# Optimization experiments

Measured on AMD Instinct MI355X. Metric: run time of the kernel, lower is better.

## Reference

```python
import jax, jax.numpy as jnp
import numpy as np

N = 6144
D_LAT = 512


def setup_inputs() -> dict:
    key = jax.random.key(0)
    k1, k2, k3 = jax.random.split(key, 3)
    latent = jax.random.normal(k1, (N, D_LAT), dtype=jnp.float32)
    coords = jax.random.normal(k2, (N, 3), dtype=jnp.float32)
    alpha = jax.random.uniform(k3, (N,), dtype=jnp.float32)
    return {"latent": latent, "coords": coords, "alpha": alpha}


def reference(latent, coords, alpha):
    # Pairwise Euclidean distances via the Gram trick (avoids [N,N,3] diff tensor).
    sq = jnp.sum(coords * coords, axis=-1)                      # [N]
    d2 = sq[:, None] + sq[None, :] - 2.0 * (coords @ coords.T)  # [N,N]
    # max with tiny eps keeps sqrt grad finite on the (zeroed-out) diagonal
    D = jnp.sqrt(jnp.maximum(d2, 1e-12)) + 1e-6                 # [N,N]
    a = 0.5 * (alpha[:, None] + alpha[None, :])                 # [N,N]
    K = jnp.clip(jnp.power(D, -a), 1e-8, 1000.0) * jnp.exp(-D / 12.0)
    K = K * (1.0 - jnp.eye(K.shape[0], dtype=K.dtype))          # zero diagonal
    K = K / (jnp.sum(K, axis=-1, keepdims=True) + 1e-8)         # row-normalize
    out = K @ latent                                            # [N,d]
    return out, K
```

## Files before the change

kernel.cpp:

```cpp
#include <hip/hip_runtime.h>
#include <hip/hip_bf16.h>

#define NN 6144
#define DLAT 512
#define SPLITK 4
#define KRANGE (NN / SPLITK)
#define KSTEPS (KRANGE / 64)
#define NROWBLK (NN / 32)
#define NWG (NROWBLK * SPLITK)

typedef __attribute__((ext_vector_type(8))) short bf16x8;
typedef __attribute__((ext_vector_type(4))) float f32x4;

#define GLOAD_LDS16(g, l) \
  __builtin_amdgcn_global_load_lds((const __attribute__((address_space(1))) unsigned int*)(g), \
                                   (__attribute__((address_space(3))) unsigned int*)(l), 16, 0, 0)

__device__ __forceinline__ float kerval(float pix, float piy, float piz, float sqi, float ahi,
                                        float4 pj, float sqj, float ahj) {
  float dot = fmaf(piz, pj.z, fmaf(piy, pj.y, pix * pj.x));
  float d2  = fmaf(-2.f, dot, sqi + sqj);
  float D   = sqrtf(fmaxf(d2, 1e-12f)) + 1e-6f;
  float a   = ahi + ahj;
  float tt  = -a * __logf(D);
  tt = fminf(fmaxf(tt, -18.420680743952367f), 6.907755278982137f);
  return __expf(fmaf(D, -1.f/12.f, tt));
}

__global__ __launch_bounds__(256) void prep_kernel(const float* __restrict__ coords,
                                                   const float* __restrict__ alpha,
                                                   float4* __restrict__ pre) {
  int j = blockIdx.x * 256 + threadIdx.x;
  if (j < NN) pre[j] = make_float4(coords[3*j], coords[3*j+1], coords[3*j+2], alpha[j]);
}

__global__ __launch_bounds__(256) void rowinv_kernel(const float4* __restrict__ pre,
                                                     float* __restrict__ inv) {
  const int i0 = blockIdx.x * 8;
  const int t = threadIdx.x;
  const int lane = t & 63;
  const int w = t >> 6;
  float4 pi[8];
  float sqi[8], ah[8], s[8];
#pragma unroll
  for (int r = 0; r < 8; ++r) {
    pi[r] = pre[i0 + r];
    sqi[r] = fmaf(pi[r].z, pi[r].z, fmaf(pi[r].y, pi[r].y, pi[r].x*pi[r].x));
    ah[r] = 0.5f * pi[r].w;
    s[r] = 0.f;
  }
  for (int j = t; j < NN; j += 256) {
    float4 pj = pre[j];
    float sqj = fmaf(pj.z, pj.z, fmaf(pj.y, pj.y, pj.x*pj.x));
    float ajh = 0.5f * pj.w;
#pragma unroll
    for (int r = 0; r < 8; ++r) {
      float v = kerval(pi[r].x, pi[r].y, pi[r].z, sqi[r], ah[r], pj, sqj, ajh);
      if (j == i0 + r) v = 0.f;
      s[r] += v;
    }
  }
#pragma unroll
  for (int r = 0; r < 8; ++r)
#pragma unroll
    for (int off = 32; off > 0; off >>= 1) s[r] += __shfl_down(s[r], off);
  __shared__ float red[8][4];
  if (lane == 0) {
#pragma unroll
    for (int r = 0; r < 8; ++r) red[r][w] = s[r];
  }
  __syncthreads();
  if (t < 8) inv[i0 + t] = 1.f / (red[t][0] + red[t][1] + red[t][2] + red[t][3] + 1e-8f);
}

__global__ __launch_bounds__(256) void btile_kernel(const float* __restrict__ latent,
                                                    __hip_bfloat16* __restrict__ BT2) {
  const int jt = blockIdx.x;
  __shared__ __hip_bfloat16 tile[32][514];
  const int t = threadIdx.x;
#pragma unroll
  for (int s = 0; s < 16; ++s) {
    int idx = s*256 + t;
    int row = idx >> 7;
    int c4  = (idx & 127) * 4;
    float4 v = *(const float4*)&latent[(size_t)(jt*32 + row)*DLAT + c4];
    tile[row][c4+0] = __float2bfloat16(v.x);
    tile[row][c4+1] = __float2bfloat16(v.y);
    tile[row][c4+2] = __float2bfloat16(v.z);
    tile[row][c4+3] = __float2bfloat16(v.w);
  }
  __syncthreads();
  const int l = t & 63;
  const int w = t >> 6;
  const int lr = (l >> 4) * 8;
  const int lc = l & 15;
#pragma unroll
  for (int cg0 = 0; cg0 < 8; ++cg0) {
    const int cg = w*8 + cg0;
    __hip_bfloat16 h[8];
#pragma unroll
    for (int q = 0; q < 8; ++q) h[q] = tile[lr + q][cg*16 + lc];
    *(bf16x8*)(BT2 + ((size_t)(jt*32 + cg)*64 + l)*8) = *(const bf16x8*)h;
  }
}

__global__ __launch_bounds__(256, 3) void fused_kernel(const float4* __restrict__ pre,
                                                       const float* __restrict__ inv,
                                                       const __hip_bfloat16* __restrict__ BT2,
                                                       float* __restrict__ Kout,
                                                       float* __restrict__ parts) {
  __shared__ __align__(16) short As[2][8][32][8];
  __shared__ __align__(16) float4 preJ[2][64];

  const int bx = blockIdx.x;
  const int wg = (bx & 7) * (NWG >> 3) + (bx >> 3);
  const int rowblk = wg % NROWBLK;
  const int z = wg / NROWBLK;
  const int rowBase = rowblk * 32;
  const int k0 = z * KRANGE;

  const int t = threadIdx.x;
  const int lane = t & 63;
  const int w = t >> 6;
  const int fr = lane & 15;
  const int fk = lane >> 4;

  const int r  = t >> 3;
  const int jg = t & 7;
  const int irow = rowBase + r;
  const float4 pi = pre[irow];
  const float sqi = fmaf(pi.z, pi.z, fmaf(pi.y, pi.y, pi.x*pi.x));
  const float ahi = 0.5f * pi.w;
  const float rinv = inv[irow];

  const int rk = rowBase - k0;
  const bool hasd = (unsigned)rk < (unsigned)KRANGE;
  const int dkt = rk >> 6;

  const int swl = ((lane & 7) << 3) | (lane >> 3);

  f32x4 acc[2][8];
#pragma unroll
  for (int m = 0; m < 2; ++m)
#pragma unroll
    for (int n = 0; n < 8; ++n) acc[m][n] = (f32x4){0.f, 0.f, 0.f, 0.f};

  if (w == 0) GLOAD_LDS16(pre + k0 + swl, &preJ[0][0]);
  __syncthreads();

  for (int kt = 0; kt < KSTEPS; ++kt) {
    const int b = kt & 1;
    const int j0 = k0 + kt * 64;

    float kv[8];
#pragma unroll
    for (int q = 0; q < 8; ++q) {
      float4 pj = preJ[b][q*8 + jg];
      float sqj = fmaf(pj.z, pj.z, fmaf(pj.y, pj.y, pj.x*pj.x));
      kv[q] = kerval(pi.x, pi.y, pi.z, sqi, ahi, pj, sqj, 0.5f*pj.w) * rinv;
    }
    if (hasd && kt == dkt) {
#pragma unroll
      for (int q = 0; q < 8; ++q)
        if (j0 + jg*8 + q == irow) kv[q] = 0.f;
    }
    {
      float* kdst = Kout + (size_t)irow * NN + j0 + jg*8;
      *(float4*)kdst       = make_float4(kv[0], kv[1], kv[2], kv[3]);
      *(float4*)(kdst + 4) = make_float4(kv[4], kv[5], kv[6], kv[7]);
      __hip_bfloat16 hb[8];
#pragma unroll
      for (int q = 0; q < 8; ++q) hb[q] = __float2bfloat16(kv[q]);
      *(bf16x8*)&As[b][jg][r][0] = *(const bf16x8*)hb;
    }
    if (w == 0 && kt + 1 < KSTEPS) GLOAD_LDS16(pre + j0 + 64 + swl, &preJ[b^1][0]);

    bf16x8 b0[8];
    {
      const size_t fb0 = ((size_t)((j0 >> 5) + 0) * 32 + w*8) * 64;
#pragma unroll
      for (int n = 0; n < 8; ++n)
        b0[n] = *(const bf16x8*)(BT2 + (fb0 + (size_t)n*64 + lane) * 8);
    }
    __syncthreads();

    bf16x8 b1[8];
    {
      const size_t fb1 = ((size_t)((j0 >> 5) + 1) * 32 + w*8) * 64;
#pragma unroll
      for (int n = 0; n < 8; ++n)
        b1[n] = *(const bf16x8*)(BT2 + (fb1 + (size_t)n*64 + lane) * 8);
    }
    {
      bf16x8 av0 = *(const bf16x8*)&As[b][fk][fr][0];
      bf16x8 av1 = *(const bf16x8*)&As[b][fk][16 + fr][0];
#pragma unroll
      for (int n = 0; n < 8; ++n) {
        acc[0][n] = __builtin_amdgcn_mfma_f32_16x16x32_bf16(av0, b0[n], acc[0][n], 0, 0, 0);
        acc[1][n] = __builtin_amdgcn_mfma_f32_16x16x32_bf16(av1, b0[n], acc[1][n], 0, 0, 0);
      }
      av0 = *(const bf16x8*)&As[b][4 + fk][fr][0];
      av1 = *(const bf16x8*)&As[b][4 + fk][16 + fr][0];
#pragma unroll
      for (int n = 0; n < 8; ++n) {
        acc[0][n] = __builtin_amdgcn_mfma_f32_16x16x32_bf16(av0, b1[n], acc[0][n], 0, 0, 0);
        acc[1][n] = __builtin_amdgcn_mfma_f32_16x16x32_bf16(av1, b1[n], acc[1][n], 0, 0, 0);
      }
    }
  }

  float* dst = parts + (size_t)z * NN * DLAT;
  const int colW = w * 128;
#pragma unroll
  for (int m = 0; m < 2; ++m)
#pragma unroll
    for (int n = 0; n < 8; ++n) {
      const int row0 = rowBase + m*16 + fk*4;
      const int c0   = colW + n*16 + fr;
#pragma unroll
      for (int i2 = 0; i2 < 4; ++i2)
        dst[(size_t)(row0 + i2)*DLAT + c0] = acc[m][n][i2];
    }
}

__global__ __launch_bounds__(256) void reduce_kernel(const float4* __restrict__ parts,
                                                     float4* __restrict__ out, int S) {
  const size_t stride = (size_t)NN * DLAT / 4;
  for (size_t idx = (size_t)blockIdx.x * 256 + threadIdx.x; idx < stride;
       idx += (size_t)gridDim.x * 256) {
    float4 a = parts[idx];
    for (int zz = 1; zz < S; ++zz) {
      float4 b = parts[idx + (size_t)zz * stride];
      a.x += b.x; a.y += b.y; a.z += b.z; a.w += b.w;
    }
    out[idx] = a;
  }
}

__global__ __launch_bounds__(256) void buildk_kernel(const float* __restrict__ coords,
                                                     const float* __restrict__ alpha,
                                                     float* __restrict__ Kout) {
  const int i = blockIdx.x;
  const int t = threadIdx.x;
  float ci0 = coords[3*i], ci1 = coords[3*i+1], ci2 = coords[3*i+2], ai = alpha[i];
  const float sqi = ci0*ci0 + ci1*ci1 + ci2*ci2;
  float vals[24];
  float lsum = 0.f;
#pragma unroll
  for (int it = 0; it < 24; ++it) {
    const int j = t + it*256;
    float c0 = coords[3*j], c1 = coords[3*j+1], c2 = coords[3*j+2], aj = alpha[j];
    float sqj = c0*c0 + c1*c1 + c2*c2;
    float dot = ci0*c0 + ci1*c1 + ci2*c2;
    float d2 = sqi + sqj - 2.f*dot;
    float D = sqrtf(fmaxf(d2, 1e-12f)) + 1e-6f;
    float a = 0.5f*(ai + aj);
    float p = __expf(-a * __logf(D));
    p = fminf(fmaxf(p, 1e-8f), 1000.f);
    float kvv = p * __expf(D * (-1.f/12.f));
    if (j == i) kvv = 0.f;
    vals[it] = kvv;
    lsum += kvv;
  }
#pragma unroll
  for (int off = 32; off > 0; off >>= 1) lsum += __shfl_down(lsum, off);
  __shared__ float red[4];
  if ((t & 63) == 0) red[t >> 6] = lsum;
  __syncthreads();
  const float inv = 1.f / (red[0] + red[1] + red[2] + red[3] + 1e-8f);
  const size_t rowoff = (size_t)i * NN;
#pragma unroll
  for (int it = 0; it < 24; ++it) Kout[rowoff + t + it*256] = vals[it] * inv;
}

__global__ __launch_bounds__(256) void gemm_fallback(const float* __restrict__ Afp,
                                                     const float* __restrict__ Bfp,
                                                     float* __restrict__ out) {
  __shared__ __align__(16) short As[2][128][72];
  __shared__ __align__(16) short Bs[2][64][72];
  const int t = threadIdx.x;
  const int rowBase = blockIdx.x * 128;
  const int colBase = blockIdx.y * 64;
  const int lane = t & 63;
  const int w  = t >> 6;
  const int wr = w >> 1;
  const int wc = w & 1;
  const int fr = lane & 15;
  const int fk = lane >> 4;
  int4 ra[4], rb[2];
  auto load_regs = [&](int kt) {
#pragma unroll
    for (int s = 0; s < 4; ++s) {
      int c = t + s*256; int rr = c >> 3, q = c & 7;
      const float* src = Afp + (size_t)(rowBase + rr)*NN + kt*64 + q*8;
      float4 f0 = *(const float4*)src;
      float4 f1 = *(const float4*)(src + 4);
      __hip_bfloat16 h[8];
      h[0]=__float2bfloat16(f0.x); h[1]=__float2bfloat16(f0.y);
      h[2]=__float2bfloat16(f0.z); h[3]=__float2bfloat16(f0.w);
      h[4]=__float2bfloat16(f1.x); h[5]=__float2bfloat16(f1.y);
      h[6]=__float2bfloat16(f1.z); h[7]=__float2bfloat16(f1.w);
      ra[s] = *(const int4*)h;
    }
#pragma unroll
    for (int s = 0; s < 2; ++s) {
      int c = t + s*256; int rr = c >> 3, q = c & 7;
      const float* src = Bfp + (size_t)(kt*64 + q*8)*DLAT + colBase + rr;
      __hip_bfloat16 h[8];
#pragma unroll
      for (int i2 = 0; i2 < 8; ++i2) h[i2] = __float2bfloat16(src[(size_t)i2*DLAT]);
      rb[s] = *(const int4*)h;
    }
  };
  auto write_tiles = [&](int buf) {
#pragma unroll
    for (int s = 0; s < 4; ++s) {
      int c = t + s*256; int rr = c >> 3, q = c & 7;
      *(int4*)&As[buf][rr][q*8] = ra[s];
    }
#pragma unroll
    for (int s = 0; s < 2; ++s) {
      int c = t + s*256; int rr = c >> 3, q = c & 7;
      *(int4*)&Bs[buf][rr][q*8] = rb[s];
    }
  };
  f32x4 acc[4][2];
#pragma unroll
  for (int m = 0; m < 4; ++m)
#pragma unroll
    for (int n = 0; n < 2; ++n) acc[m][n] = (f32x4){0.f,0.f,0.f,0.f};
  auto compute = [&](int buf) {
#pragma unroll
    for (int ks = 0; ks < 2; ++ks) {
      bf16x8 av[4], bv[2];
#pragma unroll
      for (int m = 0; m < 4; ++m) av[m] = *(const bf16x8*)&As[buf][wr*64 + m*16 + fr][ks*32 + fk*8];
#pragma unroll
      for (int n = 0; n < 2; ++n) bv[n] = *(const bf16x8*)&Bs[buf][wc*32 + n*16 + fr][ks*32 + fk*8];
#pragma unroll
      for (int m = 0; m < 4; ++m)
#pragma unroll
        for (int n = 0; n < 2; ++n)
          acc[m][n] = __builtin_amdgcn_mfma_f32_16x16x32_bf16(av[m], bv[n], acc[m][n], 0, 0, 0);
    }
  };
  load_regs(0); write_tiles(0); __syncthreads();
  int buf = 0;
  for (int kt = 0; kt < 96; ++kt) {
    if (kt + 1 < 96) load_regs(kt + 1);
    compute(buf);
    if (kt + 1 < 96) write_tiles(buf ^ 1);
    __syncthreads();
    buf ^= 1;
  }
#pragma unroll
  for (int m = 0; m < 4; ++m)
#pragma unroll
    for (int n = 0; n < 2; ++n) {
      const int row0 = rowBase + wr*64 + m*16 + fk*4;
      const int c0   = colBase + wc*32 + n*16 + fr;
#pragma unroll
      for (int i2 = 0; i2 < 4; ++i2)
        out[(size_t)(row0 + i2)*DLAT + c0] = acc[m][n][i2];
    }
}

extern "C" void kernel_launch(void* const* d_in, const int* in_sizes, int n_in,
                              void* d_out, int out_size, void* d_ws, size_t ws_size,
                              hipStream_t stream) {
  const float* latent = (const float*)d_in[0];
  const float* coords = (const float*)d_in[1];
  const float* alpha  = (const float*)d_in[2];
  float* out  = (float*)d_out;
  float* Kout = out + (size_t)NN * DLAT;

  const size_t needB = (size_t)NN * DLAT * 2;
  const size_t needP = (size_t)NN * 16;
  const size_t needI = (size_t)NN * 4;
  const size_t needS = (size_t)SPLITK * NN * DLAT * 4;

  if (ws_size >= needB + needP + needI + needS) {
    __hip_bfloat16* BT2 = (__hip_bfloat16*)d_ws;
    float4* pre  = (float4*)((char*)d_ws + needB);
    float* inv   = (float*)((char*)d_ws + needB + needP);
    float* parts = (float*)((char*)d_ws + needB + needP + needI);

    prep_kernel<<<NN/256, 256, 0, stream>>>(coords, alpha, pre);
    btile_kernel<<<NN/32, 256, 0, stream>>>(latent, BT2);
    rowinv_kernel<<<NN/8, 256, 0, stream>>>(pre, inv);
    fused_kernel<<<NWG, 256, 0, stream>>>(pre, inv, BT2, Kout, parts);
    reduce_kernel<<<768, 256, 0, stream>>>((const float4*)parts, (float4*)out, SPLITK);
  } else {
    buildk_kernel<<<NN, 256, 0, stream>>>(coords, alpha, Kout);
    gemm_fallback<<<dim3(NN/128, DLAT/64), 256, 0, stream>>>(Kout, latent, out);
  }
}
```

Before: 157.8 us.

## Hoist B-fragment loads, use nontemporal stores, explicit barrier and priority scheduling

```diff
diff --git a/kernel.cpp b/kernel.cpp
--- a/kernel.cpp
+++ b/kernel.cpp
@@ -11,10 +11,6 @@
 
 typedef __attribute__((ext_vector_type(8))) short bf16x8;
 typedef __attribute__((ext_vector_type(4))) float f32x4;
-
-#define GLOAD_LDS16(g, l) \
-  __builtin_amdgcn_global_load_lds((const __attribute__((address_space(1))) unsigned int*)(g), \
-                                   (__attribute__((address_space(3))) unsigned int*)(l), 16, 0, 0)
 
 __device__ __forceinline__ float kerval(float pix, float piy, float piz, float sqi, float ahi,
                                         float4 pj, float sqj, float ahj) {
@@ -139,18 +135,31 @@
 
   const int swl = ((lane & 7) << 3) | (lane >> 3);
 
+  const __hip_bfloat16* bbase = BT2 + ((size_t)(k0 >> 5) * 32 + w * 8) * 512 + lane * 8;
+  float* kp = Kout + (size_t)irow * NN + k0 + jg * 8;
+
   f32x4 acc[2][8];
 #pragma unroll
   for (int m = 0; m < 2; ++m)
 #pragma unroll
     for (int n = 0; n < 8; ++n) acc[m][n] = (f32x4){0.f, 0.f, 0.f, 0.f};
 
-  if (w == 0) GLOAD_LDS16(pre + k0 + swl, &preJ[0][0]);
+  if (w == 0) preJ[0][lane] = pre[k0 + swl];
   __syncthreads();
 
   for (int kt = 0; kt < KSTEPS; ++kt) {
     const int b = kt & 1;
     const int j0 = k0 + kt * 64;
+
+    bf16x8 b0[8], b1[8];
+#pragma unroll
+    for (int n = 0; n < 8; ++n) b0[n] = *(const bf16x8*)(bbase + n * 512);
+#pragma unroll
+    for (int n = 0; n < 8; ++n) b1[n] = *(const bf16x8*)(bbase + 16384 + n * 512);
+    bbase += 32768;
+
+    float4 pj_stage;
+    if (w == 0 && kt + 1 < KSTEPS) pj_stage = pre[j0 + 64 + swl];
 
     float kv[8];
 #pragma unroll
@@ -165,32 +174,27 @@
         if (j0 + jg*8 + q == irow) kv[q] = 0.f;
     }
     {
-      float* kdst = Kout + (size_t)irow * NN + j0 + jg*8;
-      *(float4*)kdst       = make_float4(kv[0], kv[1], kv[2], kv[3]);
-      *(float4*)(kdst + 4) = make_float4(kv[4], kv[5], kv[6], kv[7]);
+      f32x4 v0 = {kv[0], kv[1], kv[2], kv[3]};
+      f32x4 v1 = {kv[4], kv[5], kv[6], kv[7]};
+      __builtin_nontemporal_store(v0, (f32x4*)kp);
+      __builtin_nontemporal_store(v1, (f32x4*)(kp + 4));
+    }
+    kp += 64;
+    {
       __hip_bfloat16 hb[8];
 #pragma unroll
       for (int q = 0; q < 8; ++q) hb[q] = __float2bfloat16(kv[q]);
       *(bf16x8*)&As[b][jg][r][0] = *(const bf16x8*)hb;
     }
-    if (w == 0 && kt + 1 < KSTEPS) GLOAD_LDS16(pre + j0 + 64 + swl, &preJ[b^1][0]);
-
-    bf16x8 b0[8];
-    {
-      const size_t fb0 = ((size_t)((j0 >> 5) + 0) * 32 + w*8) * 64;
-#pragma unroll
-      for (int n = 0; n < 8; ++n)
-        b0[n] = *(const bf16x8*)(BT2 + (fb0 + (size_t)n*64 + lane) * 8);
-    }
-    __syncthreads();
-
-    bf16x8 b1[8];
-    {
-      const size_t fb1 = ((size_t)((j0 >> 5) + 1) * 32 + w*8) * 64;
-#pragma unroll
-      for (int n = 0; n < 8; ++n)
-        b1[n] = *(const bf16x8*)(BT2 + (fb1 + (size_t)n*64 + lane) * 8);
-    }
+    if (w == 0 && kt + 1 < KSTEPS) preJ[b ^ 1][lane] = pj_stage;
+
+    __builtin_amdgcn_sched_barrier(0);
+    asm volatile("s_waitcnt lgkmcnt(0)" ::: "memory");
+    __builtin_amdgcn_sched_barrier(0);
+    __builtin_amdgcn_s_barrier();
+    __builtin_amdgcn_sched_barrier(0);
+
+    __builtin_amdgcn_s_setprio(1);
     {
       bf16x8 av0 = *(const bf16x8*)&As[b][fk][fr][0];
       bf16x8 av1 = *(const bf16x8*)&As[b][fk][16 + fr][0];
@@ -207,6 +211,7 @@
         acc[1][n] = __builtin_amdgcn_mfma_f32_16x16x32_bf16(av1, b1[n], acc[1][n], 0, 0, 0);
       }
     }
+    __builtin_amdgcn_s_setprio(0);
   }
 
   float* dst = parts + (size_t)z * NN * DLAT;
@@ -219,21 +224,21 @@
       const int c0   = colW + n*16 + fr;
 #pragma unroll
       for (int i2 = 0; i2 < 4; ++i2)
-        dst[(size_t)(row0 + i2)*DLAT + c0] = acc[m][n][i2];
-    }
-}
-
-__global__ __launch_bounds__(256) void reduce_kernel(const float4* __restrict__ parts,
-                                                     float4* __restrict__ out, int S) {
+        __builtin_nontemporal_store(acc[m][n][i2], &dst[(size_t)(row0 + i2)*DLAT + c0]);
+    }
+}
+
+__global__ __launch_bounds__(256) void reduce_kernel(const f32x4* __restrict__ parts,
+                                                     f32x4* __restrict__ out, int S) {
   const size_t stride = (size_t)NN * DLAT / 4;
   for (size_t idx = (size_t)blockIdx.x * 256 + threadIdx.x; idx < stride;
        idx += (size_t)gridDim.x * 256) {
-    float4 a = parts[idx];
+    f32x4 a = __builtin_nontemporal_load(&parts[idx]);
     for (int zz = 1; zz < S; ++zz) {
-      float4 b = parts[idx + (size_t)zz * stride];
-      a.x += b.x; a.y += b.y; a.z += b.z; a.w += b.w;
-    }
-    out[idx] = a;
+      f32x4 bv = __builtin_nontemporal_load(&parts[idx + (size_t)zz * stride]);
+      a += bv;
+    }
+    __builtin_nontemporal_store(a, &out[idx]);
   }
 }
 
@@ -389,7 +394,7 @@
     btile_kernel<<<NN/32, 256, 0, stream>>>(latent, BT2);
     rowinv_kernel<<<NN/8, 256, 0, stream>>>(pre, inv);
     fused_kernel<<<NWG, 256, 0, stream>>>(pre, inv, BT2, Kout, parts);
-    reduce_kernel<<<768, 256, 0, stream>>>((const float4*)parts, (float4*)out, SPLITK);
+    reduce_kernel<<<1024, 256, 0, stream>>>((const f32x4*)parts, (f32x4*)out, SPLITK);
   } else {
     buildk_kernel<<<NN, 256, 0, stream>>>(coords, alpha, Kout);
     gemm_fallback<<<dim3(NN/128, DLAT/64), 256, 0, stream>>>(Kout, latent, out);
```

Result: slower. 175.9 us (+11.4%).
